# Performance work log

Measured on AMD Instinct MI355X. Metric: run time of the kernel, lower is better.

## Reference

```python
import jax, jax.numpy as jnp
import numpy as np

ALPHA = 0.2          # leaky_relu negative slope
NEG_INF = -9e15      # mask fill value (matches torch source)


def setup_inputs() -> dict:
    key = jax.random.key(0)
    k_h, k_mask, k_W, k_a = jax.random.split(key, 4)
    B, N, F_in, F_out = 4, 65536, 128, 128
    h = jax.random.normal(k_h, (B, N, F_in), dtype=jnp.float32)
    # op_mask > 0 means "mask out this neighbor" (prev/self/next)
    op_mask = jax.random.randint(k_mask, (B, N, 3), 0, 2, dtype=jnp.int32)
    # xavier_uniform-style init for params
    lim_W = 1.414 * np.sqrt(6.0 / (F_in + F_out))
    W = jax.random.uniform(k_W, (F_in, F_out), dtype=jnp.float32, minval=-lim_W, maxval=lim_W)
    lim_a = 1.414 * np.sqrt(6.0 / (2 * F_out + 1))
    a = jax.random.uniform(k_a, (2 * F_out, 1), dtype=jnp.float32, minval=-lim_a, maxval=lim_a)
    return {"h": h, "op_mask": op_mask, "W": W, "a": a}


def reference(h, op_mask, W, a):
    F_out = W.shape[1]
    Wh = jnp.matmul(h, W)                                   # [B, N, F]
    # windowed neighbors: prev (roll +1), self, next (roll -1)
    Wh_concat = jnp.stack(
        [jnp.roll(Wh, 1, axis=1), Wh, jnp.roll(Wh, -1, axis=1)], axis=-2
    )                                                       # [B, N, 3, F]
    Wh1 = jnp.matmul(Wh, a[:F_out])                         # [B, N, 1]
    Wh2 = jnp.matmul(Wh, a[F_out:])                         # [B, N, 1]
    Wh2_concat = jnp.stack(
        [jnp.roll(Wh2, 1, axis=1), Wh2, jnp.roll(Wh2, -1, axis=1)], axis=-1
    )                                                       # [B, N, 1, 3]
    e = jax.nn.leaky_relu(Wh1[..., None] + Wh2_concat, ALPHA)  # [B, N, 1, 3]
    e = jnp.where(op_mask[:, :, None, :] > 0, jnp.float32(NEG_INF), e)
    attention = jax.nn.softmax(e, axis=-1)                  # [B, N, 1, 3]
    # dropout_prob = 0.0 (eval-equivalent), so dropout is identity
    h_new = jnp.matmul(attention, Wh_concat).squeeze(-2)    # [B, N, F]
    return h_new
```

## Files before the change

kernel.cpp:

```cpp
#include <hip/hip_runtime.h>
#include <hip/hip_bf16.h>

typedef __attribute__((ext_vector_type(8))) short short8;
typedef __attribute__((ext_vector_type(4))) float f32x4;

#define ALPHA 0.2f
#define NEG_INF -9e15f
#define QB 14
#define NB 4
#define NN 65536
#define TPB 4682
#define TTOT (TPB * NB)
#define NBLK 512
#define WPB 8
#define NWAVES (NBLK * WPB)

__device__ __forceinline__ short fb(float x) {
    __hip_bfloat16 b = __float2bfloat16(x);
    return __builtin_bit_cast(short, b);
}
__device__ __forceinline__ float bf2f(unsigned short x) {
    union { unsigned int u; float f; } v; v.u = ((unsigned int)x) << 16;
    return v.f;
}

__global__ __launch_bounds__(256) void prep_w(const float* __restrict__ W,
                                              const float* __restrict__ a,
                                              unsigned short* __restrict__ ws) {
    const int t = threadIdx.x;
    if (blockIdx.x < 8) {
        int qg = blockIdx.x * 256 + t;
        int lane = qg & 63, f = qg >> 6;
        int kk = f >> 3, ni = f & 7;
        int slot = kk * 9 + ni;
        int n = ni * 16 + (lane & 15);
        int k0 = kk * 32 + ((lane >> 4) & 3) * 8;
        short8 o;
        #pragma unroll
        for (int j = 0; j < 8; ++j) o[j] = fb(W[(k0 + j) * 128 + n]);
        *(short8*)(ws + (size_t)(slot * 64 + lane) * 8) = o;
    } else {
        __shared__ float wa[2][128];
        {
            int k = t >> 1, sel = t & 1;
            const f32x4* wr4 = (const f32x4*)(W + k * 128);
            const f32x4* av4 = (const f32x4*)(a + sel * 128);
            float s = 0.f;
            #pragma unroll
            for (int c4 = 0; c4 < 32; ++c4) {
                f32x4 wv = wr4[c4], av = av4[c4];
                s += wv[0]*av[0] + wv[1]*av[1] + wv[2]*av[2] + wv[3]*av[3];
            }
            wa[sel][k] = s;
        }
        __syncthreads();
        {
            int lane = t & 63, kk = t >> 6;
            int l15 = lane & 15, lg = (lane >> 4) & 3;
            int k0 = kk * 32 + lg * 8;
            int slot = kk * 9 + 8;
            short8 o;
            #pragma unroll
            for (int j = 0; j < 8; ++j) o[j] = fb((l15 < 2) ? wa[l15][k0 + j] : 0.f);
            *(short8*)(ws + (size_t)(slot * 64 + lane) * 8) = o;
        }
    }
}

__global__ __launch_bounds__(512)
void gat_fused(const float* __restrict__ h, const int* __restrict__ opm,
               const unsigned short* __restrict__ ws, float* __restrict__ out) {
    __shared__ __align__(16) char Btab[36864];
    __shared__ __align__(16) char strip[WPB][4096];
    __shared__ float whs[WPB][32];
    __shared__ int   msk[WPB][44];

    const int t = threadIdx.x;
    const int lane = t & 63;
    const int w = t >> 6;
    const int l15 = lane & 15;
    const int lg = (lane >> 4) & 3;

    #pragma unroll
    for (int i = 0; i < 5; ++i) {
        int idx = t + i * 512;
        if (idx < 2304) ((f32x4*)Btab)[idx] = ((const f32x4*)ws)[idx];
    }
    __syncthreads();
    const short8* Bt = (const short8*)Btab;
    char* st = strip[w];

    for (int wt = blockIdx.x * WPB + w; wt < TTOT; wt += NWAVES) {
        const int b = wt / TPB;
        const int tt = wt - b * TPB;
        const int out0 = tt * QB;
        const int orows = min(QB, NN - out0);
        const int base = out0 - 1;
        const char* hB = (const char*)(h + (size_t)b * NN * 128);
        float* outB = out + (size_t)b * NN * 128;

        int g = base + l15;
        if (g < 0) g += NN; else if (g >= NN) g -= NN;
        const char* rp = hB + (size_t)g * 512 + (lg << 5);
        f32x4 al[4][2];
        #pragma unroll
        for (int kk = 0; kk < 4; ++kk) {
            al[kk][0] = *(const f32x4*)(rp + (kk << 7));
            al[kk][1] = *(const f32x4*)(rp + (kk << 7) + 16);
        }
        if (lane < 42) {
            int mi_ = out0 * 3 + lane;
            if (mi_ > NN * 3 - 1) mi_ = NN * 3 - 1;
            msk[w][lane] = opm[(size_t)b * (NN * 3) + mi_];
        }

        f32x4 acc[8];
        f32x4 acc2 = (f32x4){0.f, 0.f, 0.f, 0.f};
        #pragma unroll
        for (int ni = 0; ni < 8; ++ni) acc[ni] = (f32x4){0.f, 0.f, 0.f, 0.f};
        #pragma unroll
        for (int kk = 0; kk < 4; ++kk) {
            short8 av;
            av[0] = fb(al[kk][0][0]); av[1] = fb(al[kk][0][1]);
            av[2] = fb(al[kk][0][2]); av[3] = fb(al[kk][0][3]);
            av[4] = fb(al[kk][1][0]); av[5] = fb(al[kk][1][1]);
            av[6] = fb(al[kk][1][2]); av[7] = fb(al[kk][1][3]);
            #pragma unroll
            for (int ni = 0; ni < 8; ++ni)
                acc[ni] = __builtin_amdgcn_mfma_f32_16x16x32_bf16(
                    av, Bt[(kk * 9 + ni) * 64 + lane], acc[ni], 0, 0, 0);
            acc2 = __builtin_amdgcn_mfma_f32_16x16x32_bf16(
                av, Bt[(kk * 9 + 8) * 64 + lane], acc2, 0, 0, 0);
        }

        #pragma unroll
        for (int ni = 0; ni < 8; ++ni) {
            int col = (ni << 4) + l15;
            #pragma unroll
            for (int j = 0; j < 4; ++j) {
                int row = (lg << 2) + j;
                *(unsigned short*)(st + row * 256 + ((col << 1) ^ ((row & 4) << 4))) =
                    (unsigned short)fb(acc[ni][j]);
            }
        }
        if (l15 < 2) {
            #pragma unroll
            for (int j = 0; j < 4; ++j)
                whs[w][((lg << 2) + j) * 2 + l15] = acc2[j];
        }

        #pragma unroll
        for (int it = 0; it < 7; ++it) {
            int rr = (it << 1) + (lane >> 5);
            if (rr >= orows) continue;
            int r = rr + 1;
            int mk0 = msk[w][rr * 3];
            int mk1 = msk[w][rr * 3 + 1];
            int mk2 = msk[w][rr * 3 + 2];
            float w1 = whs[w][r * 2];
            float e0 = w1 + whs[w][(r - 1) * 2 + 1];
            float e1 = w1 + whs[w][r * 2 + 1];
            float e2 = w1 + whs[w][(r + 1) * 2 + 1];
            e0 = e0 > 0.f ? e0 : ALPHA * e0;
            e1 = e1 > 0.f ? e1 : ALPHA * e1;
            e2 = e2 > 0.f ? e2 : ALPHA * e2;
            if (mk0 > 0) e0 = NEG_INF;
            if (mk1 > 0) e1 = NEG_INF;
            if (mk2 > 0) e2 = NEG_INF;
            float m = fmaxf(e0, fmaxf(e1, e2));
            float x0 = __expf(e0 - m), x1 = __expf(e1 - m), x2 = __expf(e2 - m);
            float inv = 1.f / (x0 + x1 + x2);
            float a0 = x0 * inv, a1 = x1 * inv, a2 = x2 * inv;
            int cb = (lane & 31) << 3;
            ushort4 wm = *(const ushort4*)(st + (r - 1) * 256 + (cb ^ (((r - 1) & 4) << 4)));
            ushort4 w0 = *(const ushort4*)(st + r * 256 + (cb ^ ((r & 4) << 4)));
            ushort4 wp = *(const ushort4*)(st + (r + 1) * 256 + (cb ^ (((r + 1) & 4) << 4)));
            f32x4 res;
            res[0] = a0 * bf2f(wm.x) + a1 * bf2f(w0.x) + a2 * bf2f(wp.x);
            res[1] = a0 * bf2f(wm.y) + a1 * bf2f(w0.y) + a2 * bf2f(wp.y);
            res[2] = a0 * bf2f(wm.z) + a1 * bf2f(w0.z) + a2 * bf2f(wp.z);
            res[3] = a0 * bf2f(wm.w) + a1 * bf2f(w0.w) + a2 * bf2f(wp.w);
            *(f32x4*)(outB + (size_t)(out0 + rr) * 128 + ((lane & 31) << 2)) = res;
        }
    }
}

extern "C" void kernel_launch(void* const* d_in, const int* in_sizes, int n_in,
                              void* d_out, int out_size, void* d_ws, size_t ws_size,
                              hipStream_t stream) {
    const float* h   = (const float*)d_in[0];
    const int*   opm = (const int*)d_in[1];
    const float* W   = (const float*)d_in[2];
    const float* a   = (const float*)d_in[3];
    float* out = (float*)d_out;
    unsigned short* ws = (unsigned short*)d_ws;
    prep_w<<<9, 256, 0, stream>>>(W, a, ws);
    gat_fused<<<NBLK, 512, 0, stream>>>(h, opm, ws, out);
}
```

Before: 70.06 us.

## Software-prefetch next tile's h rows and mask into registers

Loads the h rows and op_mask values for the wave's next tile into registers right after converting the current tile to bf16. This lets the global loads overlap the MFMA, the LDS strip writes and the softmax epilogue instead of stalling at the top of each iteration. A sched_barrier stops the compiler from sinking the prefetch loads. The cost is extra register pressure (8 f32x4 plus the bf16 copies live at once), which could lower occupancy at 512 threads per block.

```diff
diff --git a/kernel.cpp b/kernel.cpp
--- a/kernel.cpp
+++ b/kernel.cpp
@@ -90,29 +90,69 @@
     const short8* Bt = (const short8*)Btab;
     char* st = strip[w];
 
+    f32x4 al[4][2];
+    int mreg = 0;
+    {
+        int wt = blockIdx.x * WPB + w;
+        if (wt < TTOT) {
+            int b = wt / TPB;
+            int tt = wt - b * TPB;
+            int out0 = tt * QB;
+            int g = out0 - 1 + l15;
+            if (g < 0) g += NN; else if (g >= NN) g -= NN;
+            const char* rp = (const char*)(h + (size_t)b * NN * 128) +
+                             (size_t)g * 512 + (lg << 5);
+            #pragma unroll
+            for (int kk = 0; kk < 4; ++kk) {
+                al[kk][0] = *(const f32x4*)(rp + (kk << 7));
+                al[kk][1] = *(const f32x4*)(rp + (kk << 7) + 16);
+            }
+            if (lane < 42) {
+                int mi_ = out0 * 3 + lane;
+                if (mi_ > NN * 3 - 1) mi_ = NN * 3 - 1;
+                mreg = opm[(size_t)b * (NN * 3) + mi_];
+            }
+        }
+    }
+
     for (int wt = blockIdx.x * WPB + w; wt < TTOT; wt += NWAVES) {
         const int b = wt / TPB;
         const int tt = wt - b * TPB;
         const int out0 = tt * QB;
         const int orows = min(QB, NN - out0);
-        const int base = out0 - 1;
-        const char* hB = (const char*)(h + (size_t)b * NN * 128);
         float* outB = out + (size_t)b * NN * 128;
 
-        int g = base + l15;
-        if (g < 0) g += NN; else if (g >= NN) g -= NN;
-        const char* rp = hB + (size_t)g * 512 + (lg << 5);
-        f32x4 al[4][2];
+        short8 av[4];
         #pragma unroll
         for (int kk = 0; kk < 4; ++kk) {
-            al[kk][0] = *(const f32x4*)(rp + (kk << 7));
-            al[kk][1] = *(const f32x4*)(rp + (kk << 7) + 16);
-        }
-        if (lane < 42) {
-            int mi_ = out0 * 3 + lane;
-            if (mi_ > NN * 3 - 1) mi_ = NN * 3 - 1;
-            msk[w][lane] = opm[(size_t)b * (NN * 3) + mi_];
-        }
+            av[kk][0] = fb(al[kk][0][0]); av[kk][1] = fb(al[kk][0][1]);
+            av[kk][2] = fb(al[kk][0][2]); av[kk][3] = fb(al[kk][0][3]);
+            av[kk][4] = fb(al[kk][1][0]); av[kk][5] = fb(al[kk][1][1]);
+            av[kk][6] = fb(al[kk][1][2]); av[kk][7] = fb(al[kk][1][3]);
+        }
+        if (lane < 42) msk[w][lane] = mreg;
+
+        const int wt2 = wt + NWAVES;
+        if (wt2 < TTOT) {
+            int b2 = wt2 / TPB;
+            int tt2 = wt2 - b2 * TPB;
+            int out02 = tt2 * QB;
+            int g2 = out02 - 1 + l15;
+            if (g2 < 0) g2 += NN; else if (g2 >= NN) g2 -= NN;
+            const char* rp2 = (const char*)(h + (size_t)b2 * NN * 128) +
+                              (size_t)g2 * 512 + (lg << 5);
+            #pragma unroll
+            for (int kk = 0; kk < 4; ++kk) {
+                al[kk][0] = *(const f32x4*)(rp2 + (kk << 7));
+                al[kk][1] = *(const f32x4*)(rp2 + (kk << 7) + 16);
+            }
+            if (lane < 42) {
+                int mi_ = out02 * 3 + lane;
+                if (mi_ > NN * 3 - 1) mi_ = NN * 3 - 1;
+                mreg = opm[(size_t)b2 * (NN * 3) + mi_];
+            }
+        }
+        __builtin_amdgcn_sched_barrier(0);
 
         f32x4 acc[8];
         f32x4 acc2 = (f32x4){0.f, 0.f, 0.f, 0.f};
@@ -120,17 +160,12 @@
         for (int ni = 0; ni < 8; ++ni) acc[ni] = (f32x4){0.f, 0.f, 0.f, 0.f};
         #pragma unroll
         for (int kk = 0; kk < 4; ++kk) {
-            short8 av;
-            av[0] = fb(al[kk][0][0]); av[1] = fb(al[kk][0][1]);
-            av[2] = fb(al[kk][0][2]); av[3] = fb(al[kk][0][3]);
-            av[4] = fb(al[kk][1][0]); av[5] = fb(al[kk][1][1]);
-            av[6] = fb(al[kk][1][2]); av[7] = fb(al[kk][1][3]);
             #pragma unroll
             for (int ni = 0; ni < 8; ++ni)
                 acc[ni] = __builtin_amdgcn_mfma_f32_16x16x32_bf16(
-                    av, Bt[(kk * 9 + ni) * 64 + lane], acc[ni], 0, 0, 0);
+                    av[kk], Bt[(kk * 9 + ni) * 64 + lane], acc[ni], 0, 0, 0);
             acc2 = __builtin_amdgcn_mfma_f32_16x16x32_bf16(
-                av, Bt[(kk * 9 + 8) * 64 + lane], acc2, 0, 0, 0);
+                av[kk], Bt[(kk * 9 + 8) * 64 + lane], acc2, 0, 0, 0);
         }
 
         #pragma unroll
```

Result: faster. 60.85 us (-13.1%).
